# Kernel optimization log

Hardware: AMD Instinct MI355X
Metric: run time of the kernel (lower is better)

## Reference

```python
import jax, jax.numpy as jnp
import numpy as np

B, N, F_IN, F_OUT = 8, 2048, 64, 64
ALPHA = 0.2
NEG = -9e15


def setup_inputs() -> dict:
    key = jax.random.key(0)
    k1, k2, k3, k4 = jax.random.split(key, 4)
    h = jax.random.normal(k1, (B, N, F_IN), dtype=jnp.float32)
    adj = jax.random.randint(k2, (N, N), 0, 2).astype(jnp.float32)
    W = jax.random.normal(k3, (F_OUT, F_IN), dtype=jnp.float32) * 0.05
    a = jax.random.normal(k4, (2 * F_OUT,), dtype=jnp.float32) * 0.05
    return {"h": h, "adj": adj, "W": W, "a": a}


def reference(h, adj, W, a):
    # Wh = h @ W^T  : [B, N, F_OUT]
    Wh = jnp.einsum("bnf,of->bno", h, W)
    # a([Wh_i, Wh_j]) decomposes exactly into a1.Wh_i + a2.Wh_j
    e1 = Wh @ a[:F_OUT]          # [B, N] contribution of source node i
    e2 = Wh @ a[F_OUT:]          # [B, N] contribution of target node j
    e = jax.nn.leaky_relu(e1[:, :, None] + e2[:, None, :], negative_slope=ALPHA)
    att = jnp.where(adj[None, :, :] > 0, e, NEG)
    att = jax.nn.softmax(att, axis=-1)   # [B, N, N]
    h_prime = jnp.einsum("bij,bjo->bio", att, Wh)
    return jax.nn.elu(h_prime)
```

## Files before the change

### kernel.cpp

```cpp
#include <hip/hip_runtime.h>
#include <hip/hip_bf16.h>
#include <math.h>


#define NN 2048
#define BB 8
#define ALPHA 0.2f

typedef __attribute__((ext_vector_type(8))) short s8v;
typedef __attribute__((ext_vector_type(4))) float f4v;

static __device__ __forceinline__ unsigned short bf16rne(float x) {
  union { float f; unsigned u; } c; c.f = x;
  unsigned r = c.u + 0x7FFFu + ((c.u >> 16) & 1u);
  return (unsigned short)(r >> 16);
}

__global__ __launch_bounds__(256) void k_adj(const float* __restrict__ adj,
                                             unsigned* __restrict__ adjw) {
  const int row = blockIdx.x;
  const int w = threadIdx.x >> 6, lane = threadIdx.x & 63;
  #pragma unroll
  for (int it = 0; it < 8; ++it) {
    const int j = it * 256 + w * 64 + lane;
    unsigned long long m = __ballot(adj[(size_t)row * NN + j] > 0.f);
    if (lane < 2)
      adjw[row * (NN / 32) + it * 8 + w * 2 + lane] = (unsigned)(m >> (32 * lane));
  }
}

__global__ __launch_bounds__(256) void k_wh(
    const float* __restrict__ h, const float* __restrict__ W,
    const float* __restrict__ a, unsigned short* __restrict__ whtg,
    float* __restrict__ e1, float* __restrict__ e2) {
  __shared__ __align__(16) float hsAll[64][68];
  __shared__ __align__(16) unsigned short Ws[64][72];
  const int t = threadIdx.x, lane = t & 63, w = t >> 6;
  const int rowBase = blockIdx.x * 64;
  const int b = rowBase >> 11, n0 = rowBase & (NN - 1);

  float wr[64];
  #pragma unroll
  for (int k = 0; k < 16; ++k)
    *(f4v*)&wr[k * 4] = *(const f4v*)&W[lane * 64 + k * 4];

  #pragma unroll
  for (int qq = 0; qq < 4; ++qq) {
    const int f4i = t + 256 * qq;
    const int r = f4i >> 4, c = (f4i & 15) * 4;
    *(f4v*)&hsAll[r][c] = *(const f4v*)&h[(size_t)(rowBase + r) * 64 + c];
  }
  const float a1v = a[lane], a2v = a[64 + lane];
  __syncthreads();

  #pragma unroll
  for (int g = 0; g < 4; ++g) {
    const int r0 = w * 16 + g * 4;
    float ac0 = 0.f, ac1 = 0.f, ac2 = 0.f, ac3 = 0.f;
    #pragma unroll
    for (int f4i = 0; f4i < 16; ++f4i) {
      const f4v h0 = *(const f4v*)&hsAll[r0 + 0][f4i * 4];
      const f4v h1 = *(const f4v*)&hsAll[r0 + 1][f4i * 4];
      const f4v h2 = *(const f4v*)&hsAll[r0 + 2][f4i * 4];
      const f4v h3 = *(const f4v*)&hsAll[r0 + 3][f4i * 4];
      #pragma unroll
      for (int x = 0; x < 4; ++x) {
        const float wv = wr[f4i * 4 + x];
        ac0 = fmaf(h0[x], wv, ac0);
        ac1 = fmaf(h1[x], wv, ac1);
        ac2 = fmaf(h2[x], wv, ac2);
        ac3 = fmaf(h3[x], wv, ac3);
      }
    }
    Ws[lane][r0 + 0] = bf16rne(ac0);
    Ws[lane][r0 + 1] = bf16rne(ac1);
    Ws[lane][r0 + 2] = bf16rne(ac2);
    Ws[lane][r0 + 3] = bf16rne(ac3);
    float s10 = ac0 * a1v, s20 = ac0 * a2v;
    float s11 = ac1 * a1v, s21 = ac1 * a2v;
    float s12 = ac2 * a1v, s22 = ac2 * a2v;
    float s13 = ac3 * a1v, s23 = ac3 * a2v;
    #pragma unroll
    for (int m = 1; m < 64; m <<= 1) {
      s10 += __shfl_xor(s10, m); s20 += __shfl_xor(s20, m);
      s11 += __shfl_xor(s11, m); s21 += __shfl_xor(s21, m);
      s12 += __shfl_xor(s12, m); s22 += __shfl_xor(s22, m);
      s13 += __shfl_xor(s13, m); s23 += __shfl_xor(s23, m);
    }
    if (lane == 0) {
      e1[rowBase + r0 + 0] = s10; e2[rowBase + r0 + 0] = s20;
      e1[rowBase + r0 + 1] = s11; e2[rowBase + r0 + 1] = s21;
      e1[rowBase + r0 + 2] = s12; e2[rowBase + r0 + 2] = s22;
      e1[rowBase + r0 + 3] = s13; e2[rowBase + r0 + 3] = s23;
    }
  }
  __syncthreads();

  const int o = t >> 2, seg = t & 3;
  const s8v v0 = *(const s8v*)&Ws[o][seg * 16];
  const s8v v1 = *(const s8v*)&Ws[o][seg * 16 + 8];
  unsigned short* dst = whtg + (size_t)(b * 64 + o) * NN + n0 + seg * 16;
  *(s8v*)dst = v0;
  *(s8v*)(dst + 8) = v1;
}

__global__ __launch_bounds__(256) void k_attn(
    const unsigned* __restrict__ adjw, const unsigned short* __restrict__ whtg,
    const float* __restrict__ e1g, const float* __restrict__ e2g,
    float* __restrict__ out) {
  __shared__ __align__(16) unsigned short Whs[2][64][72];
  __shared__ __align__(16) unsigned short Pts[2][32][72];
  __shared__ float e2row[NN];
  __shared__ float ls[32];

  const int t = threadIdx.x, lane = t & 63, w = t >> 6;
  const int q = lane >> 4, l15 = lane & 15;
  const int b = blockIdx.y;
  const int i0 = blockIdx.x * 32;
  const size_t bN = (size_t)b * NN;

  #pragma unroll
  for (int k = 0; k < 2; ++k) {
    const int idx = (t + 256 * k) * 4;
    *(f4v*)&e2row[idx] = *(const f4v*)&e2g[bN + idx];
  }

  const int iP = t >> 3, ocP = t & 7;
  const float e1v = e1g[bN + i0 + iP];
  const unsigned* arow = adjw + (size_t)(i0 + iP) * (NN / 32);

  f4v acc0 = {0.f, 0.f, 0.f, 0.f}, acc1 = {0.f, 0.f, 0.f, 0.f};
  float psum = 0.f;
  s8v whr0, whr1;

  auto prefetch = [&](int jt) {
    const int j0 = jt * 64;
    const int o0 = t >> 3, j80 = t & 7;
    whr0 = *(const s8v*)(whtg + (size_t)(b * 64 + o0) * NN + j0 + j80 * 8);
    const int i1 = t + 256, o1 = i1 >> 3, j81 = i1 & 7;
    whr1 = *(const s8v*)(whtg + (size_t)(b * 64 + o1) * NN + j0 + j81 * 8);
  };

  auto stage = [&](int buf, int jt) {
    const int j0 = jt * 64;
    { const int o = t >> 3, j8 = t & 7; *(s8v*)&Whs[buf][o][j8 * 8] = whr0; }
    { const int i1 = t + 256, o = i1 >> 3, j8 = i1 & 7; *(s8v*)&Whs[buf][o][j8 * 8] = whr1; }
    const unsigned wb = arow[(j0 >> 5) + (ocP >> 2)] >> ((ocP & 3) * 8);
    s8v prow;
    #pragma unroll
    for (int jj = 0; jj < 8; ++jj) {
      const float s = e1v + e2row[j0 + ocP * 8 + jj];
      const float lr = fmaxf(s, ALPHA * s);
      const float p = ((wb >> jj) & 1u) ? __expf(lr) : 0.f;
      psum += p;
      prow[jj] = (short)bf16rne(p);
    }
    *(s8v*)&Pts[buf][iP][ocP * 8] = prow;
  };

  prefetch(0);
  __syncthreads();
  stage(0, 0);
  __syncthreads();

  for (int jt = 0; jt < 32; ++jt) {
    const int cur = jt & 1;
    if (jt < 31) prefetch(jt + 1);
    #pragma unroll
    for (int ks = 0; ks < 2; ++ks) {
      const s8v bfr = *(const s8v*)&Whs[cur][w * 16 + l15][ks * 32 + q * 8];
      const s8v af0 = *(const s8v*)&Pts[cur][l15][ks * 32 + q * 8];
      const s8v af1 = *(const s8v*)&Pts[cur][16 + l15][ks * 32 + q * 8];
      acc0 = __builtin_amdgcn_mfma_f32_16x16x32_bf16(af0, bfr, acc0, 0, 0, 0);
      acc1 = __builtin_amdgcn_mfma_f32_16x16x32_bf16(af1, bfr, acc1, 0, 0, 0);
    }
    if (jt < 31) stage(cur ^ 1, jt + 1);
    __syncthreads();
  }

  psum += __shfl_xor(psum, 1);
  psum += __shfl_xor(psum, 2);
  psum += __shfl_xor(psum, 4);
  if (ocP == 0) ls[iP] = psum;
  __syncthreads();

  #pragma unroll
  for (int m = 0; m < 2; ++m) {
    const f4v av = m ? acc1 : acc0;
    #pragma unroll
    for (int r = 0; r < 4; ++r) {
      const int il = m * 16 + q * 4 + r;
      float v = av[r] / ls[il];
      v = v > 0.f ? v : expm1f(v);
      out[(bN + i0 + il) * 64 + w * 16 + l15] = v;
    }
  }
}

extern "C" void kernel_launch(void* const* d_in, const int* in_sizes, int n_in,
                              void* d_out, int out_size, void* d_ws, size_t ws_size,
                              hipStream_t stream) {
  (void)in_sizes; (void)n_in; (void)out_size; (void)ws_size;
  const float* h   = (const float*)d_in[0];
  const float* adj = (const float*)d_in[1];
  const float* W   = (const float*)d_in[2];
  const float* a   = (const float*)d_in[3];
  float* outp = (float*)d_out;

  unsigned short* whtg = (unsigned short*)d_ws;
  float* e1 = (float*)((char*)d_ws + (size_t)BB * 64 * NN * 2);
  float* e2 = e1 + (size_t)BB * NN;
  unsigned* adjw = (unsigned*)(e2 + (size_t)BB * NN);

  k_adj<<<NN, 256, 0, stream>>>(adj, adjw);
  k_wh<<<(BB * NN) / 64, 256, 0, stream>>>(h, W, a, whtg, e1, e2);
  k_attn<<<dim3(NN / 32, BB), 256, 0, stream>>>(adjw, whtg, e1, e2, outp);
}
```

Before: 104.4 us.

## Merge preprocessing kernels and rewrite attention as LDS-free single-wave blocks

Folds the adjacency bit-packing and the Wh/e1/e2 projection into one kernel launched with 512 threads, using block-index ranges to pick the role. The attention kernel becomes one wavefront per 16 rows. Each lane builds its bf16 probability fragments in registers and loads Wh MFMA operands straight from global memory, removing shared-memory staging and per-tile barriers. This saves a launch and the sync overhead, at the cost of redundant global/L2 reads of Wh across many small blocks and possible exposed load latency.

```diff
diff --git a/kernel.cpp b/kernel.cpp
--- a/kernel.cpp
+++ b/kernel.cpp
@@ -10,33 +10,33 @@
 typedef __attribute__((ext_vector_type(8))) short s8v;
 typedef __attribute__((ext_vector_type(4))) float f4v;
 
-static __device__ __forceinline__ unsigned short bf16rne(float x) {
-  union { float f; unsigned u; } c; c.f = x;
-  unsigned r = c.u + 0x7FFFu + ((c.u >> 16) & 1u);
-  return (unsigned short)(r >> 16);
-}
-
-__global__ __launch_bounds__(256) void k_adj(const float* __restrict__ adj,
-                                             unsigned* __restrict__ adjw) {
-  const int row = blockIdx.x;
-  const int w = threadIdx.x >> 6, lane = threadIdx.x & 63;
-  #pragma unroll
-  for (int it = 0; it < 8; ++it) {
-    const int j = it * 256 + w * 64 + lane;
-    unsigned long long m = __ballot(adj[(size_t)row * NN + j] > 0.f);
-    if (lane < 2)
-      adjw[row * (NN / 32) + it * 8 + w * 2 + lane] = (unsigned)(m >> (32 * lane));
-  }
-}
-
-__global__ __launch_bounds__(256) void k_wh(
-    const float* __restrict__ h, const float* __restrict__ W,
-    const float* __restrict__ a, unsigned short* __restrict__ whtg,
+static __device__ __forceinline__ unsigned pk_bf16(float lo, float hi) {
+  __hip_bfloat162 t = __float22bfloat162_rn(float2{lo, hi});
+  return *(unsigned*)&t;
+}
+
+__global__ __launch_bounds__(512) void k_pre(
+    const float* __restrict__ adj, const float* __restrict__ h,
+    const float* __restrict__ W, const float* __restrict__ a,
+    unsigned long long* __restrict__ adjq, unsigned short* __restrict__ whtg,
     float* __restrict__ e1, float* __restrict__ e2) {
+  const int t = threadIdx.x, lane = t & 63, w = t >> 6;
+
+  if (blockIdx.x < 1024) {
+    const int row = blockIdx.x * 2 + (w >> 2);
+    const int wq = w & 3;
+    #pragma unroll
+    for (int it = 0; it < 8; ++it) {
+      const int j = wq * 512 + it * 64 + lane;
+      unsigned long long m = __ballot(adj[(size_t)row * NN + j] > 0.f);
+      if (lane == 0) adjq[row * 32 + wq * 8 + it] = m;
+    }
+    return;
+  }
+
   __shared__ __align__(16) float hsAll[64][68];
   __shared__ __align__(16) unsigned short Ws[64][72];
-  const int t = threadIdx.x, lane = t & 63, w = t >> 6;
-  const int rowBase = blockIdx.x * 64;
+  const int rowBase = (blockIdx.x - 1024) * 64;
   const int b = rowBase >> 11, n0 = rowBase & (NN - 1);
 
   float wr[64];
@@ -45,156 +45,147 @@
     *(f4v*)&wr[k * 4] = *(const f4v*)&W[lane * 64 + k * 4];
 
   #pragma unroll
-  for (int qq = 0; qq < 4; ++qq) {
-    const int f4i = t + 256 * qq;
-    const int r = f4i >> 4, c = (f4i & 15) * 4;
+  for (int qq = 0; qq < 2; ++qq) {
+    const int idx = t + 512 * qq;
+    const int r = idx >> 4, c = (idx & 15) * 4;
     *(f4v*)&hsAll[r][c] = *(const f4v*)&h[(size_t)(rowBase + r) * 64 + c];
   }
   const float a1v = a[lane], a2v = a[64 + lane];
   __syncthreads();
 
-  #pragma unroll
-  for (int g = 0; g < 4; ++g) {
-    const int r0 = w * 16 + g * 4;
-    float ac0 = 0.f, ac1 = 0.f, ac2 = 0.f, ac3 = 0.f;
-    #pragma unroll
-    for (int f4i = 0; f4i < 16; ++f4i) {
-      const f4v h0 = *(const f4v*)&hsAll[r0 + 0][f4i * 4];
-      const f4v h1 = *(const f4v*)&hsAll[r0 + 1][f4i * 4];
-      const f4v h2 = *(const f4v*)&hsAll[r0 + 2][f4i * 4];
-      const f4v h3 = *(const f4v*)&hsAll[r0 + 3][f4i * 4];
-      #pragma unroll
-      for (int x = 0; x < 4; ++x) {
-        const float wv = wr[f4i * 4 + x];
-        ac0 = fmaf(h0[x], wv, ac0);
-        ac1 = fmaf(h1[x], wv, ac1);
-        ac2 = fmaf(h2[x], wv, ac2);
-        ac3 = fmaf(h3[x], wv, ac3);
-      }
-    }
-    Ws[lane][r0 + 0] = bf16rne(ac0);
-    Ws[lane][r0 + 1] = bf16rne(ac1);
-    Ws[lane][r0 + 2] = bf16rne(ac2);
-    Ws[lane][r0 + 3] = bf16rne(ac3);
-    float s10 = ac0 * a1v, s20 = ac0 * a2v;
-    float s11 = ac1 * a1v, s21 = ac1 * a2v;
-    float s12 = ac2 * a1v, s22 = ac2 * a2v;
-    float s13 = ac3 * a1v, s23 = ac3 * a2v;
-    #pragma unroll
-    for (int m = 1; m < 64; m <<= 1) {
-      s10 += __shfl_xor(s10, m); s20 += __shfl_xor(s20, m);
-      s11 += __shfl_xor(s11, m); s21 += __shfl_xor(s21, m);
-      s12 += __shfl_xor(s12, m); s22 += __shfl_xor(s22, m);
-      s13 += __shfl_xor(s13, m); s23 += __shfl_xor(s23, m);
-    }
-    if (lane == 0) {
-      e1[rowBase + r0 + 0] = s10; e2[rowBase + r0 + 0] = s20;
-      e1[rowBase + r0 + 1] = s11; e2[rowBase + r0 + 1] = s21;
-      e1[rowBase + r0 + 2] = s12; e2[rowBase + r0 + 2] = s22;
-      e1[rowBase + r0 + 3] = s13; e2[rowBase + r0 + 3] = s23;
-    }
-  }
+  const int r0 = w * 8;
+  float acc[8];
+  #pragma unroll
+  for (int rr = 0; rr < 8; ++rr) acc[rr] = 0.f;
+  #pragma unroll
+  for (int f4i = 0; f4i < 16; ++f4i) {
+    f4v hv[8];
+    #pragma unroll
+    for (int rr = 0; rr < 8; ++rr) hv[rr] = *(const f4v*)&hsAll[r0 + rr][f4i * 4];
+    #pragma unroll
+    for (int x = 0; x < 4; ++x) {
+      const float wv = wr[f4i * 4 + x];
+      #pragma unroll
+      for (int rr = 0; rr < 8; ++rr) acc[rr] = fmaf(hv[rr][x], wv, acc[rr]);
+    }
+  }
+  #pragma unroll
+  for (int p = 0; p < 4; ++p)
+    *(unsigned*)&Ws[lane][r0 + p * 2] = pk_bf16(acc[p * 2], acc[p * 2 + 1]);
+
+  float s1[8], s2[8];
+  #pragma unroll
+  for (int rr = 0; rr < 8; ++rr) { s1[rr] = acc[rr] * a1v; s2[rr] = acc[rr] * a2v; }
+  #pragma unroll
+  for (int m = 1; m < 64; m <<= 1)
+    #pragma unroll
+    for (int rr = 0; rr < 8; ++rr) {
+      s1[rr] += __shfl_xor(s1[rr], m);
+      s2[rr] += __shfl_xor(s2[rr], m);
+    }
+  if (lane == 0)
+    #pragma unroll
+    for (int rr = 0; rr < 8; ++rr) {
+      e1[rowBase + r0 + rr] = s1[rr];
+      e2[rowBase + r0 + rr] = s2[rr];
+    }
   __syncthreads();
 
-  const int o = t >> 2, seg = t & 3;
-  const s8v v0 = *(const s8v*)&Ws[o][seg * 16];
-  const s8v v1 = *(const s8v*)&Ws[o][seg * 16 + 8];
-  unsigned short* dst = whtg + (size_t)(b * 64 + o) * NN + n0 + seg * 16;
-  *(s8v*)dst = v0;
-  *(s8v*)(dst + 8) = v1;
-}
-
-__global__ __launch_bounds__(256) void k_attn(
-    const unsigned* __restrict__ adjw, const unsigned short* __restrict__ whtg,
+  const int o = t >> 3, seg = t & 7;
+  const s8v v = *(const s8v*)&Ws[o][seg * 8];
+  *(s8v*)(whtg + ((size_t)(b * 64 + o) << 11) + n0 + seg * 8) = v;
+}
+
+__global__ __launch_bounds__(64) void k_attn(
+    const unsigned long long* __restrict__ adjq,
+    const unsigned short* __restrict__ whtg,
     const float* __restrict__ e1g, const float* __restrict__ e2g,
     float* __restrict__ out) {
-  __shared__ __align__(16) unsigned short Whs[2][64][72];
-  __shared__ __align__(16) unsigned short Pts[2][32][72];
-  __shared__ float e2row[NN];
-  __shared__ float ls[32];
-
-  const int t = threadIdx.x, lane = t & 63, w = t >> 6;
+  const int lane = threadIdx.x;
   const int q = lane >> 4, l15 = lane & 15;
   const int b = blockIdx.y;
-  const int i0 = blockIdx.x * 32;
+  const int i0 = blockIdx.x * 16;
   const size_t bN = (size_t)b * NN;
 
-  #pragma unroll
-  for (int k = 0; k < 2; ++k) {
-    const int idx = (t + 256 * k) * 4;
-    *(f4v*)&e2row[idx] = *(const f4v*)&e2g[bN + idx];
-  }
-
-  const int iP = t >> 3, ocP = t & 7;
-  const float e1v = e1g[bN + i0 + iP];
-  const unsigned* arow = adjw + (size_t)(i0 + iP) * (NN / 32);
-
-  f4v acc0 = {0.f, 0.f, 0.f, 0.f}, acc1 = {0.f, 0.f, 0.f, 0.f};
+  const float e1v = e1g[bN + i0 + l15];
+  const unsigned long long* arow = adjq + (size_t)(i0 + l15) * 32;
+  const unsigned short* wb = whtg + ((size_t)b << 17);
+
+  f4v acc[4];
+  #pragma unroll
+  for (int s = 0; s < 4; ++s) acc[s] = f4v{0.f, 0.f, 0.f, 0.f};
   float psum = 0.f;
-  s8v whr0, whr1;
-
-  auto prefetch = [&](int jt) {
+
+  unsigned long long am = arow[0];
+  f4v e2r[4];
+  #pragma unroll
+  for (int ks = 0; ks < 2; ++ks)
+    #pragma unroll
+    for (int hh = 0; hh < 2; ++hh)
+      e2r[ks * 2 + hh] = *(const f4v*)&e2g[bN + ks * 32 + q * 8 + hh * 4];
+
+  for (int jt = 0; jt < 32; ++jt) {
     const int j0 = jt * 64;
-    const int o0 = t >> 3, j80 = t & 7;
-    whr0 = *(const s8v*)(whtg + (size_t)(b * 64 + o0) * NN + j0 + j80 * 8);
-    const int i1 = t + 256, o1 = i1 >> 3, j81 = i1 & 7;
-    whr1 = *(const s8v*)(whtg + (size_t)(b * 64 + o1) * NN + j0 + j81 * 8);
-  };
-
-  auto stage = [&](int buf, int jt) {
-    const int j0 = jt * 64;
-    { const int o = t >> 3, j8 = t & 7; *(s8v*)&Whs[buf][o][j8 * 8] = whr0; }
-    { const int i1 = t + 256, o = i1 >> 3, j8 = i1 & 7; *(s8v*)&Whs[buf][o][j8 * 8] = whr1; }
-    const unsigned wb = arow[(j0 >> 5) + (ocP >> 2)] >> ((ocP & 3) * 8);
-    s8v prow;
-    #pragma unroll
-    for (int jj = 0; jj < 8; ++jj) {
-      const float s = e1v + e2row[j0 + ocP * 8 + jj];
-      const float lr = fmaxf(s, ALPHA * s);
-      const float p = ((wb >> jj) & 1u) ? __expf(lr) : 0.f;
-      psum += p;
-      prow[jj] = (short)bf16rne(p);
-    }
-    *(s8v*)&Pts[buf][iP][ocP * 8] = prow;
-  };
-
-  prefetch(0);
-  __syncthreads();
-  stage(0, 0);
-  __syncthreads();
-
-  for (int jt = 0; jt < 32; ++jt) {
-    const int cur = jt & 1;
-    if (jt < 31) prefetch(jt + 1);
+    s8v bfr[8];
+    #pragma unroll
+    for (int s = 0; s < 4; ++s)
+      #pragma unroll
+      for (int ks = 0; ks < 2; ++ks)
+        bfr[s * 2 + ks] =
+            *(const s8v*)(wb + (((size_t)(s * 16 + l15)) << 11) + j0 + ks * 32 + q * 8);
+
+    s8v af[2];
     #pragma unroll
     for (int ks = 0; ks < 2; ++ks) {
-      const s8v bfr = *(const s8v*)&Whs[cur][w * 16 + l15][ks * 32 + q * 8];
-      const s8v af0 = *(const s8v*)&Pts[cur][l15][ks * 32 + q * 8];
-      const s8v af1 = *(const s8v*)&Pts[cur][16 + l15][ks * 32 + q * 8];
-      acc0 = __builtin_amdgcn_mfma_f32_16x16x32_bf16(af0, bfr, acc0, 0, 0, 0);
-      acc1 = __builtin_amdgcn_mfma_f32_16x16x32_bf16(af1, bfr, acc1, 0, 0, 0);
-    }
-    if (jt < 31) stage(cur ^ 1, jt + 1);
-    __syncthreads();
-  }
-
-  psum += __shfl_xor(psum, 1);
-  psum += __shfl_xor(psum, 2);
-  psum += __shfl_xor(psum, 4);
-  if (ocP == 0) ls[iP] = psum;
-  __syncthreads();
-
-  #pragma unroll
-  for (int m = 0; m < 2; ++m) {
-    const f4v av = m ? acc1 : acc0;
+      const unsigned bits = (unsigned)(am >> (ks * 32 + q * 8)) & 0xffu;
+      float p[8];
+      #pragma unroll
+      for (int jj = 0; jj < 8; ++jj) {
+        const float s = e1v + e2r[ks * 2 + (jj >> 2)][jj & 3];
+        const float lr = fmaxf(s, ALPHA * s);
+        const float pv = ((bits >> jj) & 1u) ? __expf(lr) : 0.f;
+        p[jj] = pv;
+        psum += pv;
+      }
+      union { s8v v; unsigned u[4]; } cv;
+      cv.u[0] = pk_bf16(p[0], p[1]);
+      cv.u[1] = pk_bf16(p[2], p[3]);
+      cv.u[2] = pk_bf16(p[4], p[5]);
+      cv.u[3] = pk_bf16(p[6], p[7]);
+      af[ks] = cv.v;
+    }
+
+    if (jt < 31) {
+      am = arow[jt + 1];
+      const int jn = j0 + 64;
+      #pragma unroll
+      for (int ks = 0; ks < 2; ++ks)
+        #pragma unroll
+        for (int hh = 0; hh < 2; ++hh)
+          e2r[ks * 2 + hh] = *(const f4v*)&e2g[bN + jn + ks * 32 + q * 8 + hh * 4];
+    }
+
+    #pragma unroll
+    for (int s = 0; s < 4; ++s) {
+      acc[s] = __builtin_amdgcn_mfma_f32_16x16x32_bf16(af[0], bfr[s * 2 + 0], acc[s], 0, 0, 0);
+      acc[s] = __builtin_amdgcn_mfma_f32_16x16x32_bf16(af[1], bfr[s * 2 + 1], acc[s], 0, 0, 0);
+    }
+  }
+
+  psum += __shfl_xor(psum, 16);
+  psum += __shfl_xor(psum, 32);
+  float rs[4];
+  #pragma unroll
+  for (int r = 0; r < 4; ++r) rs[r] = __shfl(psum, q * 4 + r);
+
+  #pragma unroll
+  for (int s = 0; s < 4; ++s)
     #pragma unroll
     for (int r = 0; r < 4; ++r) {
-      const int il = m * 16 + q * 4 + r;
-      float v = av[r] / ls[il];
+      float v = acc[s][r] / rs[r];
       v = v > 0.f ? v : expm1f(v);
-      out[(bN + i0 + il) * 64 + w * 16 + l15] = v;
-    }
-  }
+      out[(bN + i0 + q * 4 + r) * 64 + s * 16 + l15] = v;
+    }
 }
 
 extern "C" void kernel_launch(void* const* d_in, const int* in_sizes, int n_in,
@@ -210,9 +201,8 @@
   unsigned short* whtg = (unsigned short*)d_ws;
   float* e1 = (float*)((char*)d_ws + (size_t)BB * 64 * NN * 2);
   float* e2 = e1 + (size_t)BB * NN;
-  unsigned* adjw = (unsigned*)(e2 + (size_t)BB * NN);
-
-  k_adj<<<NN, 256, 0, stream>>>(adj, adjw);
-  k_wh<<<(BB * NN) / 64, 256, 0, stream>>>(h, W, a, whtg, e1, e2);
-  k_attn<<<dim3(NN / 32, BB), 256, 0, stream>>>(adjw, whtg, e1, e2, outp);
-}
+  unsigned long long* adjq = (unsigned long long*)(e2 + (size_t)BB * NN);
+
+  k_pre<<<1280, 512, 0, stream>>>(adj, h, W, a, adjq, whtg, e1, e2);
+  k_attn<<<dim3(NN / 16, BB), 64, 0, stream>>>(adjq, whtg, e1, e2, outp);
+}
```

Measured after the change: 125.6 us. 20.3% more time.
